# Optimization experiments

Hardware: AMD Instinct MI355X
Metric: run time of the kernel (lower is better)

## Reference

```python
import jax, jax.numpy as jnp
import numpy as np

N_USER = 100000
N_ITEM = 100000
E = 1600000
B = 16384
D = 128
LAYERS = [128, 128]
NEG_SLOPE = 0.2
EPS = 1e-12


def _l2norm(x):
    # F.normalize(x, dim=1, p=2): x / max(||x||, eps)
    n = jnp.sqrt(jnp.sum(x * x, axis=1, keepdims=True))
    return x / jnp.maximum(n, EPS)


def _sage_layer(h, src, dst, W_self, W_neigh, b):
    # DGL SAGEConv('mean'): mean-aggregate neighbor feats, then
    # fc_self(h) + fc_neigh(h_neigh) + bias
    msg = h[src]                                   # [E, D_in] gather
    agg = jax.ops.segment_sum(msg, dst, num_segments=h.shape[0])
    deg = jax.ops.segment_sum(jnp.ones((src.shape[0],), h.dtype), dst,
                              num_segments=h.shape[0])
    h_neigh = agg / jnp.maximum(deg, 1.0)[:, None]  # zero in-degree -> 0
    out = h @ W_self + h_neigh @ W_neigh + b
    return jax.nn.leaky_relu(out, NEG_SLOPE)


def setup_inputs() -> dict:
    key = jax.random.key(0)
    ks = jax.random.split(key, 20)
    inp = {}
    inp["src"] = jax.random.randint(ks[0], (E,), 0, N_USER)
    inp["dst"] = jax.random.randint(ks[1], (E,), 0, N_USER)
    inp["users"] = jax.random.randint(ks[2], (B,), 0, N_USER)
    inp["pos_items"] = jax.random.randint(ks[3], (B,), 0, N_ITEM)
    inp["neg_items"] = jax.random.randint(ks[4], (B,), 0, N_ITEM)
    inp["user_feat"] = jax.random.normal(ks[5], (N_USER, D), jnp.float32) * 0.05
    inp["item_feat"] = jax.random.normal(ks[6], (N_ITEM, D), jnp.float32) * 0.05
    dims = [D] + LAYERS
    i = 7
    for l in range(len(LAYERS)):
        di, do = dims[l], dims[l + 1]
        s = 1.0 / np.sqrt(di)
        inp[f"Wu_self{l}"] = jax.random.normal(ks[i], (di, do), jnp.float32) * s; i += 1
        inp[f"Wu_neigh{l}"] = jax.random.normal(ks[i], (di, do), jnp.float32) * s; i += 1
        inp[f"bu{l}"] = jnp.zeros((do,), jnp.float32)
        inp[f"Wi{l}"] = jax.random.normal(ks[i], (di, do), jnp.float32) * s; i += 1
        inp[f"bi{l}"] = jnp.zeros((do,), jnp.float32)
    return inp


def reference(src, dst, users, pos_items, neg_items, user_feat, item_feat,
              Wu_self0, Wu_neigh0, bu0, Wi0, bi0,
              Wu_self1, Wu_neigh1, bu1, Wi1, bi1):
    user_params = [(Wu_self0, Wu_neigh0, bu0), (Wu_self1, Wu_neigh1, bu1)]
    item_params = [(Wi0, bi0), (Wi1, bi1)]

    h_u = user_feat
    user_embeds = [h_u]
    for (Ws, Wn, b) in user_params:
        h_u = _sage_layer(h_u, src, dst, Ws, Wn, b)
        h_u = _l2norm(h_u)  # dropout p=0 -> identity
        user_embeds.append(h_u)

    h_i = item_feat
    item_embeds = [h_i]
    for (W, b) in item_params:
        h_i = jax.nn.leaky_relu(h_i @ W + b, NEG_SLOPE)
        h_i = _l2norm(h_i)
        item_embeds.append(h_i)

    user_embd = jnp.concatenate(user_embeds, axis=1)   # [N_user, 3*D]
    item_embd = jnp.concatenate(item_embeds, axis=1)   # [N_item, 3*D]

    return (user_embd[users], item_embd[pos_items], item_embd[neg_items])
```

## Files before the change

### kernel.cpp

```cpp
#include <hip/hip_runtime.h>

#define NU 100000
#define NI 100000
#define NE 1600000
#define BB 16384
#define DD 128

static constexpr int SCAN_CHUNK = 2048;
static constexpr int SCAN_NBLK  = (NU + SCAN_CHUNK - 1) / SCAN_CHUNK;
static constexpr int USER_TILES = NU / 16;

static constexpr int NXCD   = 8;
static constexpr int DRANGE = NU / NXCD;
static constexpr int K_CH   = 32;
static constexpr int CHUNK4 = NE / 4 / K_CH;
static constexpr int HIST_BLKS = NXCD * K_CH;
static constexpr int PACK_BLKS = 48;
static constexpr int CVT_UNIT  = 2048;
static constexpr int CVT_TOT   = NU * 32;
static constexpr int CVT_BLKS  = (CVT_TOT + CVT_UNIT - 1) / CVT_UNIT;

static constexpr size_t OFF_DEG      = 0;
static constexpr size_t OFF_ROWSTART = 400128;
static constexpr size_t OFF_CURSOR   = 800256;
static constexpr size_t OFF_BSUM     = 1200384;
static constexpr size_t OFF_EDGESRC  = 1200640;
static constexpr size_t OFF_H1       = 7600640;
static constexpr size_t OFF_WFRAG    = 58800640;


typedef __bf16 bf16x8 __attribute__((ext_vector_type(8)));
typedef float f32x4 __attribute__((ext_vector_type(4)));
typedef unsigned int u32x4 __attribute__((ext_vector_type(4)));

union frag_u {
    u32x4 u;
    bf16x8 b;
    unsigned short us[8];
};

__device__ __forceinline__ unsigned short f2bf(float f) {
    unsigned u = __float_as_uint(f);
    u = (u + 0x7fffu + ((u >> 16) & 1u)) >> 16;
    return (unsigned short)u;
}

__device__ __forceinline__ unsigned pack_bf16_pair(float a, float b) {
    return (unsigned)f2bf(a) | ((unsigned)f2bf(b) << 16);
}

__device__ __forceinline__ float2 unpack_bf16_pair(unsigned u) {
    float2 r;
    r.x = __uint_as_float(u << 16);
    r.y = __uint_as_float(u & 0xffff0000u);
    return r;
}

__device__ __forceinline__ f32x4 mfma16(bf16x8 a, bf16x8 b, f32x4 c) {
    return __builtin_amdgcn_mfma_f32_16x16x32_bf16(a, b, c, 0, 0, 0);
}

__device__ __forceinline__ bf16x8 bfrag(const u32x4* __restrict__ wf, int idx) {
    frag_u f;
    f.u = wf[idx];
    return f.b;
}

__device__ __forceinline__ void make_afrag_hilo(const float* rowp, int kb,
                                                bf16x8* hi, bf16x8* lo) {
    float4 v0 = *(const float4*)(rowp + kb);
    float4 v1 = *(const float4*)(rowp + kb + 4);
    float vv[8] = {v0.x, v0.y, v0.z, v0.w, v1.x, v1.y, v1.z, v1.w};
    frag_u h, l;
    #pragma unroll
    for (int e = 0; e < 8; ++e) {
        unsigned short hb = f2bf(vv[e]);
        h.us[e] = hb;
        float hf = __uint_as_float(((unsigned)hb) << 16);
        l.us[e] = f2bf(vv[e] - hf);
    }
    *hi = h.b;
    *lo = l.b;
}

__global__ __launch_bounds__(256) void mega_prep(
    const int* __restrict__ dst, int* __restrict__ hist,
    const float* __restrict__ uf, unsigned* __restrict__ ubf,
    const float* __restrict__ Ws0, const float* __restrict__ Wn0,
    const float* __restrict__ Ws1, const float* __restrict__ Wn1,
    const float* __restrict__ Wi0, const float* __restrict__ Wi1,
    u32x4* __restrict__ wfrag) {
    __shared__ int h[DRANGE];
    int t = threadIdx.x;
    if (blockIdx.x < HIST_BLKS) {
        int r = blockIdx.x & (NXCD - 1);
        int k = blockIdx.x >> 3;
        for (int j = t; j < DRANGE; j += 256) h[j] = 0;
        __syncthreads();
        int lo = r * DRANGE;
        const int4* d4 = (const int4*)dst + (size_t)k * CHUNK4;
        for (int i = t; i < CHUNK4; i += 256) {
            int4 d = d4[i];
            if ((unsigned)(d.x - lo) < (unsigned)DRANGE) atomicAdd(&h[d.x - lo], 1);
            if ((unsigned)(d.y - lo) < (unsigned)DRANGE) atomicAdd(&h[d.y - lo], 1);
            if ((unsigned)(d.z - lo) < (unsigned)DRANGE) atomicAdd(&h[d.z - lo], 1);
            if ((unsigned)(d.w - lo) < (unsigned)DRANGE) atomicAdd(&h[d.w - lo], 1);
        }
        __syncthreads();
        int* hb = hist + (size_t)(r * K_CH + k) * DRANGE;
        for (int j = t; j < DRANGE; j += 256) hb[j] = h[j];
    } else if (blockIdx.x < HIST_BLKS + PACK_BLKS) {
        int i = (blockIdx.x - HIST_BLKS) * 256 + t;
        const float* tab[6] = {Ws0, Wn0, Ws1, Wn1, Wi0, Wi1};
        int matg = i >> 11;
        int j = (i >> 8) & 7, kk = (i >> 6) & 3, ln = i & 63;
        const float* W = tab[matg];
        int n = j * 16 + (ln & 15);
        int kb = kk * 32 + (ln >> 4) * 8;
        unsigned short u[8];
        #pragma unroll
        for (int e = 0; e < 8; ++e) u[e] = f2bf(W[(size_t)(kb + e) * DD + n]);
        u32x4 w;
        w[0] = u[0] | ((unsigned)u[1] << 16);
        w[1] = u[2] | ((unsigned)u[3] << 16);
        w[2] = u[4] | ((unsigned)u[5] << 16);
        w[3] = u[6] | ((unsigned)u[7] << 16);
        wfrag[i] = w;
    } else {
        int bid2 = blockIdx.x - HIST_BLKS - PACK_BLKS;
        const float4* uf4 = (const float4*)uf;
        uint2* ub2 = (uint2*)ubf;
        #pragma unroll
        for (int it = 0; it < 8; ++it) {
            int idx = bid2 * CVT_UNIT + it * 256 + t;
            if (idx < CVT_TOT) {
                float4 v = uf4[idx];
                uint2 o;
                o.x = pack_bf16_pair(v.x, v.y);
                o.y = pack_bf16_pair(v.z, v.w);
                ub2[idx] = o;
            }
        }
    }
}

__global__ __launch_bounds__(256) void deg_reduce(const int* __restrict__ hist,
                                                  int* __restrict__ deg) {
    int d = blockIdx.x * 256 + threadIdx.x;
    if (d >= NU) return;
    int r = d / DRANGE, j = d - r * DRANGE;
    const int* hb = hist + (size_t)r * K_CH * DRANGE + j;
    int s = 0;
    #pragma unroll
    for (int k = 0; k < K_CH; ++k) s += hb[(size_t)k * DRANGE];
    deg[d] = s;
}

__global__ __launch_bounds__(256) void scan1_kernel(const int* __restrict__ deg,
                                                    int* __restrict__ bsum) {
    __shared__ int sh[256];
    int t = threadIdx.x;
    int base = blockIdx.x * SCAN_CHUNK + t * 8;
    int s = 0;
    #pragma unroll
    for (int j = 0; j < 8; ++j) {
        int idx = base + j;
        s += (idx < NU) ? deg[idx] : 0;
    }
    sh[t] = s;
    __syncthreads();
    for (int off = 128; off > 0; off >>= 1) {
        if (t < off) sh[t] += sh[t + off];
        __syncthreads();
    }
    if (t == 0) bsum[blockIdx.x] = sh[0];
}

__global__ void scan2_kernel(int* __restrict__ bsum) {
    if (threadIdx.x == 0) {
        int acc = 0;
        for (int i = 0; i < SCAN_NBLK; ++i) {
            int v = bsum[i];
            bsum[i] = acc;
            acc += v;
        }
    }
}

__global__ __launch_bounds__(256) void scan3_kernel(const int* __restrict__ deg,
                                                    const int* __restrict__ bsum,
                                                    int* __restrict__ row_start) {
    __shared__ int sh[256];
    int t = threadIdx.x;
    int base = blockIdx.x * SCAN_CHUNK + t * 8;
    int v[8];
    int s = 0;
    #pragma unroll
    for (int j = 0; j < 8; ++j) {
        int idx = base + j;
        v[j] = (idx < NU) ? deg[idx] : 0;
        s += v[j];
    }
    sh[t] = s;
    __syncthreads();
    for (int off = 1; off < 256; off <<= 1) {
        int val = sh[t];
        int add = (t >= off) ? sh[t - off] : 0;
        __syncthreads();
        sh[t] = val + add;
        __syncthreads();
    }
    int excl = sh[t] - s + bsum[blockIdx.x];
    #pragma unroll
    for (int j = 0; j < 8; ++j) {
        int idx = base + j;
        if (idx < NU) row_start[idx] = excl;
        excl += v[j];
    }
}

__global__ __launch_bounds__(256) void base_kernel(const int* __restrict__ row_start,
                                                   int* __restrict__ hist) {
    int d = blockIdx.x * 256 + threadIdx.x;
    if (d >= NU) return;
    int r = d / DRANGE, j = d - r * DRANGE;
    int* hb = hist + (size_t)r * K_CH * DRANGE + j;
    int acc = row_start[d];
    #pragma unroll
    for (int k = 0; k < K_CH; ++k) {
        int c = hb[(size_t)k * DRANGE];
        hb[(size_t)k * DRANGE] = acc;
        acc += c;
    }
}

__global__ __launch_bounds__(256) void fill2(const int* __restrict__ src,
                                             const int* __restrict__ dst,
                                             const int* __restrict__ base,
                                             int* __restrict__ edge_src) {
    __shared__ int cur[DRANGE];
    int r = blockIdx.x & (NXCD - 1);
    int k = blockIdx.x >> 3;
    int t = threadIdx.x;
    const int* bb = base + (size_t)(r * K_CH + k) * DRANGE;
    for (int j = t; j < DRANGE; j += 256) cur[j] = bb[j];
    __syncthreads();
    int lo = r * DRANGE;
    const int4* d4 = (const int4*)dst + (size_t)k * CHUNK4;
    const int4* s4 = (const int4*)src + (size_t)k * CHUNK4;
    for (int i = t; i < CHUNK4; i += 256) {
        int4 d = d4[i];
        int4 s = s4[i];
        if ((unsigned)(d.x - lo) < (unsigned)DRANGE) edge_src[atomicAdd(&cur[d.x - lo], 1)] = s.x;
        if ((unsigned)(d.y - lo) < (unsigned)DRANGE) edge_src[atomicAdd(&cur[d.y - lo], 1)] = s.y;
        if ((unsigned)(d.z - lo) < (unsigned)DRANGE) edge_src[atomicAdd(&cur[d.z - lo], 1)] = s.z;
        if ((unsigned)(d.w - lo) < (unsigned)DRANGE) edge_src[atomicAdd(&cur[d.w - lo], 1)] = s.w;
    }
}

__global__ __launch_bounds__(256) void agg_kernel(const unsigned* __restrict__ ubf,
                                                  const int* __restrict__ row_start,
                                                  const int* __restrict__ deg,
                                                  const int* __restrict__ edge_src,
                                                  unsigned* __restrict__ hn) {
    int wid = blockIdx.x * 4 + (threadIdx.x >> 6);
    int lane = threadIdx.x & 63;
    if (wid >= NU) return;
    int st = row_start[wid];
    int dg = deg[wid];
    int lanelet = lane & 15;
    int eslot = lane >> 4;
    float acc[8] = {0.f, 0.f, 0.f, 0.f, 0.f, 0.f, 0.f, 0.f};
    const unsigned* colp = ubf + (lanelet << 2);
    for (int base = 0; base < dg; base += 64) {
        int n = min(dg - base, 64);
        int myidx = (lane < n) ? edge_src[st + base + lane] : 0;
        int e = 0;
        #pragma unroll 2
        for (; e + 4 <= n; e += 4) {
            int s = __shfl(myidx, e + eslot, 64);
            u32x4 v = *(const u32x4*)(colp + (size_t)s * 64);
            #pragma unroll
            for (int k = 0; k < 4; ++k) {
                float2 f = unpack_bf16_pair(v[k]);
                acc[2 * k] += f.x;
                acc[2 * k + 1] += f.y;
            }
        }
        int rem = n - e;
        int s = __shfl(myidx, min(e + eslot, 63), 64);
        if (eslot < rem) {
            u32x4 v = *(const u32x4*)(colp + (size_t)s * 64);
            #pragma unroll
            for (int k = 0; k < 4; ++k) {
                float2 f = unpack_bf16_pair(v[k]);
                acc[2 * k] += f.x;
                acc[2 * k + 1] += f.y;
            }
        }
    }
    #pragma unroll
    for (int k = 0; k < 8; ++k) {
        acc[k] += __shfl_xor(acc[k], 16, 64);
        acc[k] += __shfl_xor(acc[k], 32, 64);
    }
    float inv = 1.0f / fmaxf((float)dg, 1.0f);
    if (eslot == 0) {
        u32x4 o;
        o[0] = pack_bf16_pair(acc[0] * inv, acc[1] * inv);
        o[1] = pack_bf16_pair(acc[2] * inv, acc[3] * inv);
        o[2] = pack_bf16_pair(acc[4] * inv, acc[5] * inv);
        o[3] = pack_bf16_pair(acc[6] * inv, acc[7] * inv);
        *(u32x4*)(hn + (size_t)wid * 64 + (lanelet << 2)) = o;
    }
}

__global__ __launch_bounds__(256) void user_mm_mfma(
    const float* __restrict__ hself, const unsigned short* __restrict__ hn,
    const u32x4* __restrict__ wf, const float* __restrict__ bias,
    float* __restrict__ out) {
    int t = threadIdx.x;
    int lane = t & 63;
    int tile = blockIdx.x * 4 + (t >> 6);
    if (tile >= USER_TILES) return;
    int gbase = tile * 16;
    int m = lane & 15, q = lane >> 4;
    const float* selfp = hself + (size_t)(gbase + m) * DD;
    const unsigned short* neighp = hn + (size_t)(gbase + m) * DD;
    bf16x8 as_hi[4], as_lo[4], an[4];
    #pragma unroll
    for (int kk = 0; kk < 4; ++kk) {
        int kb = kk * 32 + q * 8;
        make_afrag_hilo(selfp, kb, &as_hi[kk], &as_lo[kk]);
        frag_u f;
        f.u = *(const u32x4*)(neighp + kb);
        an[kk] = f.b;
    }
    f32x4 acc[8];
    f32x4 zero = {0.f, 0.f, 0.f, 0.f};
    #pragma unroll
    for (int j = 0; j < 8; ++j) acc[j] = zero;
    #pragma unroll 2
    for (int j = 0; j < 8; ++j) {
        #pragma unroll
        for (int kk = 0; kk < 4; ++kk) {
            bf16x8 bs = bfrag(wf, (j * 4 + kk) * 64 + lane);
            acc[j] = mfma16(as_hi[kk], bs, acc[j]);
            acc[j] = mfma16(as_lo[kk], bs, acc[j]);
            bf16x8 bn = bfrag(wf, 2048 + (j * 4 + kk) * 64 + lane);
            acc[j] = mfma16(an[kk], bn, acc[j]);
        }
    }
    float ss[4] = {0.f, 0.f, 0.f, 0.f};
    #pragma unroll
    for (int j = 0; j < 8; ++j) {
        float bj = bias[j * 16 + m];
        #pragma unroll
        for (int r = 0; r < 4; ++r) {
            float x = acc[j][r] + bj;
            x = x > 0.f ? x : 0.2f * x;
            acc[j][r] = x;
            ss[r] += x * x;
        }
    }
    #pragma unroll
    for (int r = 0; r < 4; ++r) {
        float s = ss[r];
        s += __shfl_xor(s, 1, 64);
        s += __shfl_xor(s, 2, 64);
        s += __shfl_xor(s, 4, 64);
        s += __shfl_xor(s, 8, 64);
        ss[r] = 1.0f / fmaxf(sqrtf(s), 1e-12f);
    }
    #pragma unroll
    for (int j = 0; j < 8; ++j)
        #pragma unroll
        for (int r = 0; r < 4; ++r)
            out[(size_t)(gbase + q * 4 + r) * DD + j * 16 + m] = acc[j][r] * ss[r];
}

__global__ __launch_bounds__(256) void tail_fuse(
    const float* __restrict__ ufeat, const float* __restrict__ h1,
    const int* __restrict__ users, const int* __restrict__ row_start,
    const int* __restrict__ deg, const int* __restrict__ edge_src,
    const float* __restrict__ ifeat, const int* __restrict__ pos,
    const int* __restrict__ neg, const u32x4* __restrict__ wf_u,
    const u32x4* __restrict__ wf_i, const float* __restrict__ bu1,
    const float* __restrict__ bi0, const float* __restrict__ bi1,
    float* __restrict__ out) {
    __shared__ float scratch[4][16 * 132];
    int t = threadIdx.x;
    int lane = t & 63, wave = t >> 6;
    int m = lane & 15, q = lane >> 4;
    f32x4 zero = {0.f, 0.f, 0.f, 0.f};

    if (blockIdx.x < 1024) {
        int gb = blockIdx.x * 16;
        float* sc = scratch[0];
        int L = lane & 31;
        int eslot = lane >> 5;
        const float* hl = h1 + 4 * L;
        #pragma unroll
        for (int rr = 0; rr < 4; ++rr) {
            int r = wave * 4 + rr;
            int u = users[gb + r];
            int st = row_start[u], dg = deg[u], en = st + dg;
            float ax = 0.f, ay = 0.f, az = 0.f, aw = 0.f;
            int e = st;
            for (; e + 4 <= en; e += 4) {
                int s0 = edge_src[e], s1 = edge_src[e + 1];
                int s2 = edge_src[e + 2], s3 = edge_src[e + 3];
                int sA = eslot ? s1 : s0;
                int sB = eslot ? s3 : s2;
                float4 vA = *(const float4*)(hl + (size_t)sA * DD);
                float4 vB = *(const float4*)(hl + (size_t)sB * DD);
                ax += vA.x + vB.x;
                ay += vA.y + vB.y;
                az += vA.z + vB.z;
                aw += vA.w + vB.w;
            }
            if (e + 2 <= en) {
                int s0 = edge_src[e], s1 = edge_src[e + 1];
                int sA = eslot ? s1 : s0;
                float4 vA = *(const float4*)(hl + (size_t)sA * DD);
                ax += vA.x;
                ay += vA.y;
                az += vA.z;
                aw += vA.w;
                e += 2;
            }
            if (e < en) {
                int s0 = edge_src[e];
                if (eslot == 0) {
                    float4 vA = *(const float4*)(hl + (size_t)s0 * DD);
                    ax += vA.x;
                    ay += vA.y;
                    az += vA.z;
                    aw += vA.w;
                }
            }
            ax += __shfl_xor(ax, 32, 64);
            ay += __shfl_xor(ay, 32, 64);
            az += __shfl_xor(az, 32, 64);
            aw += __shfl_xor(aw, 32, 64);
            float inv = 1.0f / fmaxf((float)dg, 1.0f);
            if (eslot == 0) {
                float4 o = {ax * inv, ay * inv, az * inv, aw * inv};
                *(float4*)(sc + r * 132 + 4 * L) = o;
            }
            float* orow = out + (size_t)(gb + r) * 384;
            ((float2*)orow)[lane] = ((const float2*)(ufeat + (size_t)u * DD))[lane];
            ((float2*)orow)[64 + lane] = ((const float2*)(h1 + (size_t)u * DD))[lane];
        }
        __syncthreads();
        if (wave != 0) return;
        int um = users[gb + m];
        const float* selfp = h1 + (size_t)um * DD;
        bf16x8 sh[4], sl[4], nh[4], nl[4];
        #pragma unroll
        for (int kk = 0; kk < 4; ++kk) {
            int kb = kk * 32 + q * 8;
            make_afrag_hilo(selfp, kb, &sh[kk], &sl[kk]);
            make_afrag_hilo(sc + m * 132, kb, &nh[kk], &nl[kk]);
        }
        f32x4 acc[8];
        #pragma unroll
        for (int j = 0; j < 8; ++j) acc[j] = zero;
        #pragma unroll 2
        for (int j = 0; j < 8; ++j) {
            #pragma unroll
            for (int kk = 0; kk < 4; ++kk) {
                bf16x8 bs = bfrag(wf_u, (j * 4 + kk) * 64 + lane);
                acc[j] = mfma16(sh[kk], bs, acc[j]);
                acc[j] = mfma16(sl[kk], bs, acc[j]);
                bf16x8 bn = bfrag(wf_u, 2048 + (j * 4 + kk) * 64 + lane);
                acc[j] = mfma16(nh[kk], bn, acc[j]);
                acc[j] = mfma16(nl[kk], bn, acc[j]);
            }
        }
        float ss[4] = {0.f, 0.f, 0.f, 0.f};
        #pragma unroll
        for (int j = 0; j < 8; ++j) {
            float bj = bu1[j * 16 + m];
            #pragma unroll
            for (int r = 0; r < 4; ++r) {
                float x = acc[j][r] + bj;
                x = x > 0.f ? x : 0.2f * x;
                acc[j][r] = x;
                ss[r] += x * x;
            }
        }
        #pragma unroll
        for (int r = 0; r < 4; ++r) {
            float s = ss[r];
            s += __shfl_xor(s, 1, 64);
            s += __shfl_xor(s, 2, 64);
            s += __shfl_xor(s, 4, 64);
            s += __shfl_xor(s, 8, 64);
            ss[r] = 1.0f / fmaxf(sqrtf(s), 1e-12f);
        }
        #pragma unroll
        for (int j = 0; j < 8; ++j)
            #pragma unroll
            for (int r = 0; r < 4; ++r)
                out[(size_t)(gb + q * 4 + r) * 384 + 256 + j * 16 + m] = acc[j][r] * ss[r];
        return;
    }

    int tile = (blockIdx.x - 1024) * 4 + wave;
    int gb = tile * 16;
    float* sc = scratch[wave];
    int rowm = gb + m;
    int idxm = (rowm < BB) ? pos[rowm] : neg[rowm - BB];
    const float* rowp = ifeat + (size_t)idxm * DD;
    bf16x8 ahi[4], alo[4];
    #pragma unroll
    for (int kk = 0; kk < 4; ++kk)
        make_afrag_hilo(rowp, kk * 32 + q * 8, &ahi[kk], &alo[kk]);
    f32x4 acc[8];
    #pragma unroll
    for (int j = 0; j < 8; ++j) acc[j] = zero;
    #pragma unroll 2
    for (int j = 0; j < 8; ++j) {
        #pragma unroll
        for (int kk = 0; kk < 4; ++kk) {
            bf16x8 b = bfrag(wf_i, (j * 4 + kk) * 64 + lane);
            acc[j] = mfma16(ahi[kk], b, acc[j]);
            acc[j] = mfma16(alo[kk], b, acc[j]);
        }
    }
    float ss[4] = {0.f, 0.f, 0.f, 0.f};
    #pragma unroll
    for (int j = 0; j < 8; ++j) {
        float bj = bi0[j * 16 + m];
        #pragma unroll
        for (int r = 0; r < 4; ++r) {
            float x = acc[j][r] + bj;
            x = x > 0.f ? x : 0.2f * x;
            acc[j][r] = x;
            ss[r] += x * x;
        }
    }
    #pragma unroll
    for (int r = 0; r < 4; ++r) {
        float s = ss[r];
        s += __shfl_xor(s, 1, 64);
        s += __shfl_xor(s, 2, 64);
        s += __shfl_xor(s, 4, 64);
        s += __shfl_xor(s, 8, 64);
        ss[r] = 1.0f / fmaxf(sqrtf(s), 1e-12f);
    }
    #pragma unroll
    for (int j = 0; j < 8; ++j)
        #pragma unroll
        for (int r = 0; r < 4; ++r)
            sc[(q * 4 + r) * 132 + j * 16 + m] = acc[j][r] * ss[r];
    for (int r = 0; r < 16; ++r) {
        int row = gb + r;
        int idx = (row < BB) ? pos[row] : neg[row - BB];
        float* orow = out + (size_t)(BB + row) * 384;
        ((float2*)orow)[lane] = ((const float2*)(ifeat + (size_t)idx * DD))[lane];
        float2 r1v;
        r1v.x = sc[r * 132 + 2 * lane];
        r1v.y = sc[r * 132 + 2 * lane + 1];
        ((float2*)orow)[64 + lane] = r1v;
    }
    bf16x8 chi[4], clo[4];
    #pragma unroll
    for (int kk = 0; kk < 4; ++kk)
        make_afrag_hilo(sc + m * 132, kk * 32 + q * 8, &chi[kk], &clo[kk]);
    #pragma unroll
    for (int j = 0; j < 8; ++j) acc[j] = zero;
    #pragma unroll 2
    for (int j = 0; j < 8; ++j) {
        #pragma unroll
        for (int kk = 0; kk < 4; ++kk) {
            bf16x8 b = bfrag(wf_i, 2048 + (j * 4 + kk) * 64 + lane);
            acc[j] = mfma16(chi[kk], b, acc[j]);
            acc[j] = mfma16(clo[kk], b, acc[j]);
        }
    }
    float ss1[4] = {0.f, 0.f, 0.f, 0.f};
    #pragma unroll
    for (int j = 0; j < 8; ++j) {
        float bj = bi1[j * 16 + m];
        #pragma unroll
        for (int r = 0; r < 4; ++r) {
            float x = acc[j][r] + bj;
            x = x > 0.f ? x : 0.2f * x;
            acc[j][r] = x;
            ss1[r] += x * x;
        }
    }
    #pragma unroll
    for (int r = 0; r < 4; ++r) {
        float s = ss1[r];
        s += __shfl_xor(s, 1, 64);
        s += __shfl_xor(s, 2, 64);
        s += __shfl_xor(s, 4, 64);
        s += __shfl_xor(s, 8, 64);
        ss1[r] = 1.0f / fmaxf(sqrtf(s), 1e-12f);
    }
    #pragma unroll
    for (int j = 0; j < 8; ++j)
        #pragma unroll
        for (int r = 0; r < 4; ++r)
            out[(size_t)(BB + gb + q * 4 + r) * 384 + 256 + j * 16 + m] = acc[j][r] * ss1[r];
}

extern "C" void kernel_launch(void* const* d_in, const int* in_sizes, int n_in,
                              void* d_out, int out_size, void* d_ws, size_t ws_size,
                              hipStream_t stream) {
    const int* src = (const int*)d_in[0];
    const int* dst = (const int*)d_in[1];
    const int* users = (const int*)d_in[2];
    const int* pos = (const int*)d_in[3];
    const int* neg = (const int*)d_in[4];
    const float* ufeat = (const float*)d_in[5];
    const float* ifeat = (const float*)d_in[6];
    const float* Ws0 = (const float*)d_in[7];
    const float* Wn0 = (const float*)d_in[8];
    const float* bu0 = (const float*)d_in[9];
    const float* Wi0 = (const float*)d_in[10];
    const float* bi0 = (const float*)d_in[11];
    const float* Ws1 = (const float*)d_in[12];
    const float* Wn1 = (const float*)d_in[13];
    const float* bu1 = (const float*)d_in[14];
    const float* Wi1 = (const float*)d_in[15];
    const float* bi1 = (const float*)d_in[16];
    float* out = (float*)d_out;

    char* ws = (char*)d_ws;
    int* deg = (int*)(ws + OFF_DEG);
    int* row_start = (int*)(ws + OFF_ROWSTART);
    int* bsum = (int*)(ws + OFF_BSUM);
    int* edge_src = (int*)(ws + OFF_EDGESRC);
    float* h1 = (float*)(ws + OFF_H1);
    u32x4* wfrag = (u32x4*)(ws + OFF_WFRAG);

    unsigned* ubf = (unsigned*)d_out;
    unsigned* hn = (unsigned*)((char*)d_out + (size_t)NU * DD * 2);
    int* hist = (int*)((char*)d_out + (size_t)NU * DD * 4);
    const unsigned short* hn_us = (const unsigned short*)hn;

    mega_prep<<<HIST_BLKS + PACK_BLKS + CVT_BLKS, 256, 0, stream>>>(
        dst, hist, ufeat, ubf, Ws0, Wn0, Ws1, Wn1, Wi0, Wi1, wfrag);
    deg_reduce<<<(NU + 255) / 256, 256, 0, stream>>>(hist, deg);
    scan1_kernel<<<SCAN_NBLK, 256, 0, stream>>>(deg, bsum);
    scan2_kernel<<<1, 64, 0, stream>>>(bsum);
    scan3_kernel<<<SCAN_NBLK, 256, 0, stream>>>(deg, bsum, row_start);
    base_kernel<<<(NU + 255) / 256, 256, 0, stream>>>(row_start, hist);
    fill2<<<HIST_BLKS, 256, 0, stream>>>(src, dst, hist, edge_src);
    agg_kernel<<<(NU + 3) / 4, 256, 0, stream>>>(ubf, row_start, deg, edge_src, hn);
    user_mm_mfma<<<(USER_TILES + 3) / 4, 256, 0, stream>>>(ufeat, hn_us, wfrag, bu0, h1);
    tail_fuse<<<1024 + 512, 256, 0, stream>>>(ufeat, h1, users, row_start, deg, edge_src,
                                              ifeat, pos, neg, wfrag + 4096, wfrag + 8192,
                                              bu1, bi0, bi1, out);
}
```

Before: 453.3 us.

## Split tail MFMA work across all four waves and batch edge index loads

The fused tail kernel now divides each 16-row output tile's N dimension across the four waves (two 16-column blocks each), instead of running the whole tile on one wave. Per-row norms are combined through a small shared-memory partial-sum array with block barriers. Item tiles now get one block each, so the grid grows to 2048 item blocks. The user neighbor gather loads up to 64 edge indices per wave in one coalesced load and hands them out with shuffles, instead of every lane re-reading the same indices. The cost is extra barriers and shared-memory traffic, and each wave now redundantly builds the full A fragments.

```diff
diff --git a/kernel.cpp b/kernel.cpp
--- a/kernel.cpp
+++ b/kernel.cpp
@@ -22,7 +22,6 @@
 
 static constexpr size_t OFF_DEG      = 0;
 static constexpr size_t OFF_ROWSTART = 400128;
-static constexpr size_t OFF_CURSOR   = 800256;
 static constexpr size_t OFF_BSUM     = 1200384;
 static constexpr size_t OFF_EDGESRC  = 1200640;
 static constexpr size_t OFF_H1       = 7600640;
@@ -388,7 +387,8 @@
     const u32x4* __restrict__ wf_i, const float* __restrict__ bu1,
     const float* __restrict__ bi0, const float* __restrict__ bi1,
     float* __restrict__ out) {
-    __shared__ float scratch[4][16 * 132];
+    __shared__ float sc[16 * 132];
+    __shared__ float ssp[16 * 4];
     int t = threadIdx.x;
     int lane = t & 63, wave = t >> 6;
     int m = lane & 15, q = lane >> 4;
@@ -396,7 +396,6 @@
 
     if (blockIdx.x < 1024) {
         int gb = blockIdx.x * 16;
-        float* sc = scratch[0];
         int L = lane & 31;
         int eslot = lane >> 5;
         const float* hl = h1 + 4 * L;
@@ -404,39 +403,24 @@
         for (int rr = 0; rr < 4; ++rr) {
             int r = wave * 4 + rr;
             int u = users[gb + r];
-            int st = row_start[u], dg = deg[u], en = st + dg;
+            int st = row_start[u], dg = deg[u];
             float ax = 0.f, ay = 0.f, az = 0.f, aw = 0.f;
-            int e = st;
-            for (; e + 4 <= en; e += 4) {
-                int s0 = edge_src[e], s1 = edge_src[e + 1];
-                int s2 = edge_src[e + 2], s3 = edge_src[e + 3];
-                int sA = eslot ? s1 : s0;
-                int sB = eslot ? s3 : s2;
-                float4 vA = *(const float4*)(hl + (size_t)sA * DD);
-                float4 vB = *(const float4*)(hl + (size_t)sB * DD);
-                ax += vA.x + vB.x;
-                ay += vA.y + vB.y;
-                az += vA.z + vB.z;
-                aw += vA.w + vB.w;
-            }
-            if (e + 2 <= en) {
-                int s0 = edge_src[e], s1 = edge_src[e + 1];
-                int sA = eslot ? s1 : s0;
-                float4 vA = *(const float4*)(hl + (size_t)sA * DD);
-                ax += vA.x;
-                ay += vA.y;
-                az += vA.z;
-                aw += vA.w;
-                e += 2;
-            }
-            if (e < en) {
-                int s0 = edge_src[e];
-                if (eslot == 0) {
-                    float4 vA = *(const float4*)(hl + (size_t)s0 * DD);
-                    ax += vA.x;
-                    ay += vA.y;
-                    az += vA.z;
-                    aw += vA.w;
+            for (int base = 0; base < dg; base += 64) {
+                int n = min(dg - base, 64);
+                int myidx = (lane < n) ? edge_src[st + base + lane] : 0;
+                int e = 0;
+                #pragma unroll 4
+                for (; e + 2 <= n; e += 2) {
+                    int s = __shfl(myidx, e + eslot, 64);
+                    float4 v = *(const float4*)(hl + (size_t)s * DD);
+                    ax += v.x; ay += v.y; az += v.z; aw += v.w;
+                }
+                if (e < n) {
+                    int s = __shfl(myidx, e, 64);
+                    if (eslot == 0) {
+                        float4 v = *(const float4*)(hl + (size_t)s * DD);
+                        ax += v.x; ay += v.y; az += v.z; aw += v.w;
+                    }
                 }
             }
             ax += __shfl_xor(ax, 32, 64);
@@ -453,7 +437,7 @@
             ((float2*)orow)[64 + lane] = ((const float2*)(h1 + (size_t)u * DD))[lane];
         }
         __syncthreads();
-        if (wave != 0) return;
+        int j0 = wave * 2;
         int um = users[gb + m];
         const float* selfp = h1 + (size_t)um * DD;
         bf16x8 sh[4], sl[4], nh[4], nl[4];
@@ -463,53 +447,54 @@
             make_afrag_hilo(selfp, kb, &sh[kk], &sl[kk]);
             make_afrag_hilo(sc + m * 132, kb, &nh[kk], &nl[kk]);
         }
-        f32x4 acc[8];
-        #pragma unroll
-        for (int j = 0; j < 8; ++j) acc[j] = zero;
-        #pragma unroll 2
-        for (int j = 0; j < 8; ++j) {
-            #pragma unroll
-            for (int kk = 0; kk < 4; ++kk) {
-                bf16x8 bs = bfrag(wf_u, (j * 4 + kk) * 64 + lane);
-                acc[j] = mfma16(sh[kk], bs, acc[j]);
-                acc[j] = mfma16(sl[kk], bs, acc[j]);
-                bf16x8 bn = bfrag(wf_u, 2048 + (j * 4 + kk) * 64 + lane);
-                acc[j] = mfma16(nh[kk], bn, acc[j]);
-                acc[j] = mfma16(nl[kk], bn, acc[j]);
-            }
-        }
-        float ss[4] = {0.f, 0.f, 0.f, 0.f};
-        #pragma unroll
-        for (int j = 0; j < 8; ++j) {
-            float bj = bu1[j * 16 + m];
-            #pragma unroll
-            for (int r = 0; r < 4; ++r) {
-                float x = acc[j][r] + bj;
-                x = x > 0.f ? x : 0.2f * x;
-                acc[j][r] = x;
-                ss[r] += x * x;
-            }
-        }
+        f32x4 a0 = zero, a1 = zero;
+        #pragma unroll
+        for (int kk = 0; kk < 4; ++kk) {
+            bf16x8 b0 = bfrag(wf_u, (j0 * 4 + kk) * 64 + lane);
+            a0 = mfma16(sh[kk], b0, a0);
+            a0 = mfma16(sl[kk], b0, a0);
+            bf16x8 n0 = bfrag(wf_u, 2048 + (j0 * 4 + kk) * 64 + lane);
+            a0 = mfma16(nh[kk], n0, a0);
+            a0 = mfma16(nl[kk], n0, a0);
+            bf16x8 b1 = bfrag(wf_u, ((j0 + 1) * 4 + kk) * 64 + lane);
+            a1 = mfma16(sh[kk], b1, a1);
+            a1 = mfma16(sl[kk], b1, a1);
+            bf16x8 n1 = bfrag(wf_u, 2048 + ((j0 + 1) * 4 + kk) * 64 + lane);
+            a1 = mfma16(nh[kk], n1, a1);
+            a1 = mfma16(nl[kk], n1, a1);
+        }
+        float bj0 = bu1[j0 * 16 + m], bj1 = bu1[(j0 + 1) * 16 + m];
+        float ss[4];
         #pragma unroll
         for (int r = 0; r < 4; ++r) {
-            float s = ss[r];
+            float x0 = a0[r] + bj0; x0 = x0 > 0.f ? x0 : 0.2f * x0; a0[r] = x0;
+            float x1 = a1[r] + bj1; x1 = x1 > 0.f ? x1 : 0.2f * x1; a1[r] = x1;
+            float s = x0 * x0 + x1 * x1;
             s += __shfl_xor(s, 1, 64);
             s += __shfl_xor(s, 2, 64);
             s += __shfl_xor(s, 4, 64);
             s += __shfl_xor(s, 8, 64);
-            ss[r] = 1.0f / fmaxf(sqrtf(s), 1e-12f);
-        }
-        #pragma unroll
-        for (int j = 0; j < 8; ++j)
+            ss[r] = s;
+        }
+        if (m == 0) {
             #pragma unroll
-            for (int r = 0; r < 4; ++r)
-                out[(size_t)(gb + q * 4 + r) * 384 + 256 + j * 16 + m] = acc[j][r] * ss[r];
+            for (int r = 0; r < 4; ++r) ssp[(q * 4 + r) * 4 + wave] = ss[r];
+        }
+        __syncthreads();
+        #pragma unroll
+        for (int r = 0; r < 4; ++r) {
+            int row = q * 4 + r;
+            float tot = ssp[row * 4] + ssp[row * 4 + 1] + ssp[row * 4 + 2] + ssp[row * 4 + 3];
+            float inv = 1.0f / fmaxf(sqrtf(tot), 1e-12f);
+            out[(size_t)(gb + row) * 384 + 256 + j0 * 16 + m] = a0[r] * inv;
+            out[(size_t)(gb + row) * 384 + 256 + (j0 + 1) * 16 + m] = a1[r] * inv;
+        }
         return;
     }
 
-    int tile = (blockIdx.x - 1024) * 4 + wave;
+    int tile = blockIdx.x - 1024;
     int gb = tile * 16;
-    float* sc = scratch[wave];
+    int j0 = wave * 2;
     int rowm = gb + m;
     int idxm = (rowm < BB) ? pos[rowm] : neg[rowm - BB];
     const float* rowp = ifeat + (size_t)idxm * DD;
@@ -517,45 +502,48 @@
     #pragma unroll
     for (int kk = 0; kk < 4; ++kk)
         make_afrag_hilo(rowp, kk * 32 + q * 8, &ahi[kk], &alo[kk]);
-    f32x4 acc[8];
-    #pragma unroll
-    for (int j = 0; j < 8; ++j) acc[j] = zero;
-    #pragma unroll 2
-    for (int j = 0; j < 8; ++j) {
-        #pragma unroll
-        for (int kk = 0; kk < 4; ++kk) {
-            bf16x8 b = bfrag(wf_i, (j * 4 + kk) * 64 + lane);
-            acc[j] = mfma16(ahi[kk], b, acc[j]);
-            acc[j] = mfma16(alo[kk], b, acc[j]);
-        }
-    }
-    float ss[4] = {0.f, 0.f, 0.f, 0.f};
-    #pragma unroll
-    for (int j = 0; j < 8; ++j) {
-        float bj = bi0[j * 16 + m];
+    f32x4 a0 = zero, a1 = zero;
+    #pragma unroll
+    for (int kk = 0; kk < 4; ++kk) {
+        bf16x8 b0 = bfrag(wf_i, (j0 * 4 + kk) * 64 + lane);
+        a0 = mfma16(ahi[kk], b0, a0);
+        a0 = mfma16(alo[kk], b0, a0);
+        bf16x8 b1 = bfrag(wf_i, ((j0 + 1) * 4 + kk) * 64 + lane);
+        a1 = mfma16(ahi[kk], b1, a1);
+        a1 = mfma16(alo[kk], b1, a1);
+    }
+    {
+        float bj0 = bi0[j0 * 16 + m], bj1 = bi0[(j0 + 1) * 16 + m];
+        float ss[4];
         #pragma unroll
         for (int r = 0; r < 4; ++r) {
-            float x = acc[j][r] + bj;
-            x = x > 0.f ? x : 0.2f * x;
-            acc[j][r] = x;
-            ss[r] += x * x;
-        }
-    }
-    #pragma unroll
-    for (int r = 0; r < 4; ++r) {
-        float s = ss[r];
-        s += __shfl_xor(s, 1, 64);
-        s += __shfl_xor(s, 2, 64);
-        s += __shfl_xor(s, 4, 64);
-        s += __shfl_xor(s, 8, 64);
-        ss[r] = 1.0f / fmaxf(sqrtf(s), 1e-12f);
-    }
-    #pragma unroll
-    for (int j = 0; j < 8; ++j)
-        #pragma unroll
-        for (int r = 0; r < 4; ++r)
-            sc[(q * 4 + r) * 132 + j * 16 + m] = acc[j][r] * ss[r];
-    for (int r = 0; r < 16; ++r) {
+            float x0 = a0[r] + bj0; x0 = x0 > 0.f ? x0 : 0.2f * x0; a0[r] = x0;
+            float x1 = a1[r] + bj1; x1 = x1 > 0.f ? x1 : 0.2f * x1; a1[r] = x1;
+            float s = x0 * x0 + x1 * x1;
+            s += __shfl_xor(s, 1, 64);
+            s += __shfl_xor(s, 2, 64);
+            s += __shfl_xor(s, 4, 64);
+            s += __shfl_xor(s, 8, 64);
+            ss[r] = s;
+        }
+        if (m == 0) {
+            #pragma unroll
+            for (int r = 0; r < 4; ++r) ssp[(q * 4 + r) * 4 + wave] = ss[r];
+        }
+        __syncthreads();
+        #pragma unroll
+        for (int r = 0; r < 4; ++r) {
+            int row = q * 4 + r;
+            float tot = ssp[row * 4] + ssp[row * 4 + 1] + ssp[row * 4 + 2] + ssp[row * 4 + 3];
+            float inv = 1.0f / fmaxf(sqrtf(tot), 1e-12f);
+            sc[row * 132 + j0 * 16 + m] = a0[r] * inv;
+            sc[row * 132 + (j0 + 1) * 16 + m] = a1[r] * inv;
+        }
+        __syncthreads();
+    }
+    #pragma unroll
+    for (int rr = 0; rr < 4; ++rr) {
+        int r = wave * 4 + rr;
         int row = gb + r;
         int idx = (row < BB) ? pos[row] : neg[row - BB];
         float* orow = out + (size_t)(BB + row) * 384;
@@ -569,43 +557,45 @@
     #pragma unroll
     for (int kk = 0; kk < 4; ++kk)
         make_afrag_hilo(sc + m * 132, kk * 32 + q * 8, &chi[kk], &clo[kk]);
-    #pragma unroll
-    for (int j = 0; j < 8; ++j) acc[j] = zero;
-    #pragma unroll 2
-    for (int j = 0; j < 8; ++j) {
-        #pragma unroll
-        for (int kk = 0; kk < 4; ++kk) {
-            bf16x8 b = bfrag(wf_i, 2048 + (j * 4 + kk) * 64 + lane);
-            acc[j] = mfma16(chi[kk], b, acc[j]);
-            acc[j] = mfma16(clo[kk], b, acc[j]);
-        }
-    }
-    float ss1[4] = {0.f, 0.f, 0.f, 0.f};
-    #pragma unroll
-    for (int j = 0; j < 8; ++j) {
-        float bj = bi1[j * 16 + m];
+    a0 = zero; a1 = zero;
+    #pragma unroll
+    for (int kk = 0; kk < 4; ++kk) {
+        bf16x8 b0 = bfrag(wf_i, 2048 + (j0 * 4 + kk) * 64 + lane);
+        a0 = mfma16(chi[kk], b0, a0);
+        a0 = mfma16(clo[kk], b0, a0);
+        bf16x8 b1 = bfrag(wf_i, 2048 + ((j0 + 1) * 4 + kk) * 64 + lane);
+        a1 = mfma16(chi[kk], b1, a1);
+        a1 = mfma16(clo[kk], b1, a1);
+    }
+    {
+        float bj0 = bi1[j0 * 16 + m], bj1 = bi1[(j0 + 1) * 16 + m];
+        float ss[4];
         #pragma unroll
         for (int r = 0; r < 4; ++r) {
-            float x = acc[j][r] + bj;
-            x = x > 0.f ? x : 0.2f * x;
-            acc[j][r] = x;
-            ss1[r] += x * x;
-        }
-    }
-    #pragma unroll
-    for (int r = 0; r < 4; ++r) {
-        float s = ss1[r];
-        s += __shfl_xor(s, 1, 64);
-        s += __shfl_xor(s, 2, 64);
-        s += __shfl_xor(s, 4, 64);
-        s += __shfl_xor(s, 8, 64);
-        ss1[r] = 1.0f / fmaxf(sqrtf(s), 1e-12f);
-    }
-    #pragma unroll
-    for (int j = 0; j < 8; ++j)
-        #pragma unroll
-        for (int r = 0; r < 4; ++r)
-            out[(size_t)(BB + gb + q * 4 + r) * 384 + 256 + j * 16 + m] = acc[j][r] * ss1[r];
+            float x0 = a0[r] + bj0; x0 = x0 > 0.f ? x0 : 0.2f * x0; a0[r] = x0;
+            float x1 = a1[r] + bj1; x1 = x1 > 0.f ? x1 : 0.2f * x1; a1[r] = x1;
+            float s = x0 * x0 + x1 * x1;
+            s += __shfl_xor(s, 1, 64);
+            s += __shfl_xor(s, 2, 64);
+            s += __shfl_xor(s, 4, 64);
+            s += __shfl_xor(s, 8, 64);
+            ss[r] = s;
+        }
+        __syncthreads();
+        if (m == 0) {
+            #pragma unroll
+            for (int r = 0; r < 4; ++r) ssp[(q * 4 + r) * 4 + wave] = ss[r];
+        }
+        __syncthreads();
+        #pragma unroll
+        for (int r = 0; r < 4; ++r) {
+            int row = q * 4 + r;
+            float tot = ssp[row * 4] + ssp[row * 4 + 1] + ssp[row * 4 + 2] + ssp[row * 4 + 3];
+            float inv = 1.0f / fmaxf(sqrtf(tot), 1e-12f);
+            out[(size_t)(BB + gb + row) * 384 + 256 + j0 * 16 + m] = a0[r] * inv;
+            out[(size_t)(BB + gb + row) * 384 + 256 + (j0 + 1) * 16 + m] = a1[r] * inv;
+        }
+    }
 }
 
 extern "C" void kernel_launch(void* const* d_in, const int* in_sizes, int n_in,
@@ -653,7 +643,7 @@
     fill2<<<HIST_BLKS, 256, 0, stream>>>(src, dst, hist, edge_src);
     agg_kernel<<<(NU + 3) / 4, 256, 0, stream>>>(ubf, row_start, deg, edge_src, hn);
     user_mm_mfma<<<(USER_TILES + 3) / 4, 256, 0, stream>>>(ufeat, hn_us, wfrag, bu0, h1);
-    tail_fuse<<<1024 + 512, 256, 0, stream>>>(ufeat, h1, users, row_start, deg, edge_src,
-                                              ifeat, pos, neg, wfrag + 4096, wfrag + 8192,
-                                              bu1, bi0, bi1, out);
-}
+    tail_fuse<<<1024 + 2048, 256, 0, stream>>>(ufeat, h1, users, row_start, deg, edge_src,
+                                               ifeat, pos, neg, wfrag + 4096, wfrag + 8192,
+                                               bu1, bi0, bi1, out);
+}
```

After: 440.1 us. -2.9%, faster.
